# Kernel optimization log

Measured on AMD Instinct MI355X. Metric: run time of the kernel, lower is better.

The kernel has to match this reference:

```python
import jax, jax.numpy as jnp
import numpy as np

N = 50000      # nodes
E = 800000     # edges (before self-loops)
D_IN = 256     # input feature dim
H = 4          # attention heads
C = 32         # per-head channels
HID = H * C    # 128, concat output dim
BN_EPS = 1e-5


def setup_inputs() -> dict:
    key = jax.random.key(0)
    ks = jax.random.split(key, 24)
    inp = {}
    inp["x"] = jax.random.normal(ks[0], (N, D_IN), jnp.float32)
    inp["edge_index"] = jax.random.randint(ks[1], (2, E), 0, N, jnp.int32)
    # layer 1 GATConv params
    inp["W1"] = jax.random.normal(ks[2], (D_IN, HID), jnp.float32) * (2.0 / (D_IN + HID)) ** 0.5
    inp["att_src1"] = jax.random.normal(ks[3], (H, C), jnp.float32) * 0.1
    inp["att_dst1"] = jax.random.normal(ks[4], (H, C), jnp.float32) * 0.1
    inp["bias1"] = jnp.zeros((HID,), jnp.float32)
    # layer 1 BatchNorm (eval mode)
    inp["gamma1"] = 1.0 + 0.1 * jax.random.normal(ks[5], (HID,), jnp.float32)
    inp["beta1"] = 0.1 * jax.random.normal(ks[6], (HID,), jnp.float32)
    inp["mean1"] = 0.1 * jax.random.normal(ks[7], (HID,), jnp.float32)
    inp["var1"] = 0.5 + jax.random.uniform(ks[8], (HID,), jnp.float32)
    # layer 2 GATConv params
    inp["W2"] = jax.random.normal(ks[9], (HID, HID), jnp.float32) * (2.0 / (HID + HID)) ** 0.5
    inp["att_src2"] = jax.random.normal(ks[10], (H, C), jnp.float32) * 0.1
    inp["att_dst2"] = jax.random.normal(ks[11], (H, C), jnp.float32) * 0.1
    inp["bias2"] = jnp.zeros((HID,), jnp.float32)
    # layer 2 BatchNorm (eval mode)
    inp["gamma2"] = 1.0 + 0.1 * jax.random.normal(ks[12], (HID,), jnp.float32)
    inp["beta2"] = 0.1 * jax.random.normal(ks[13], (HID,), jnp.float32)
    inp["mean2"] = 0.1 * jax.random.normal(ks[14], (HID,), jnp.float32)
    inp["var2"] = 0.5 + jax.random.uniform(ks[15], (HID,), jnp.float32)
    return inp


def _gat_layer(x, src, dst, W, att_src, att_dst, bias):
    # x: [N, D]; src/dst: [Etot] with self-loops already appended
    h = (x @ W).reshape(N, H, C)                       # [N, H, C]
    a_s = jnp.einsum("nhc,hc->nh", h, att_src)         # [N, H]
    a_d = jnp.einsum("nhc,hc->nh", h, att_dst)         # [N, H]
    e = jax.nn.leaky_relu(a_s[src] + a_d[dst], 0.2)    # [Etot, H]
    # edge softmax over incoming edges of each destination node
    m = jax.ops.segment_max(e, dst, num_segments=N)    # [N, H]
    ex = jnp.exp(e - m[dst])                           # [Etot, H]
    den = jax.ops.segment_sum(ex, dst, num_segments=N) # [N, H]
    alpha = ex / (den[dst] + 1e-16)                    # [Etot, H]
    out = jax.ops.segment_sum(h[src] * alpha[:, :, None], dst, num_segments=N)
    return out.reshape(N, HID) + bias                  # concat heads + bias


def _bn_eval(x, gamma, beta, mean, var):
    return (x - mean) * (gamma * jax.lax.rsqrt(var + BN_EPS)) + beta


def reference(x, edge_index, W1, att_src1, att_dst1, bias1, gamma1, beta1, mean1, var1,
              W2, att_src2, att_dst2, bias2, gamma2, beta2, mean2, var2):
    loop = jnp.arange(N, dtype=edge_index.dtype)
    src = jnp.concatenate([edge_index[0], loop])  # PyG GATConv adds self-loops
    dst = jnp.concatenate([edge_index[1], loop])
    h = _gat_layer(x, src, dst, W1, att_src1, att_dst1, bias1)
    h = jax.nn.relu(_bn_eval(h, gamma1, beta1, mean1, var1))  # dropout = identity (eval)
    h = _gat_layer(h, src, dst, W2, att_src2, att_dst2, bias2)
    h = jax.nn.relu(_bn_eval(h, gamma2, beta2, mean2, var2))
    return h
```

## Files before the change

kernel.cpp:

```cpp
#include <hip/hip_runtime.h>
#include <math.h>

#define N_NODES 50000
#define EDGES   800000
#define ETOT    (EDGES + N_NODES)
#define HID     128
#define NH      4

typedef __attribute__((ext_vector_type(8))) short short8;
typedef __attribute__((ext_vector_type(4))) float floatx4;

__device__ inline unsigned short f2bf(float f) {
    unsigned int u = __float_as_uint(f);
    u = u + 0x7FFFu + ((u >> 16) & 1u);
    return (unsigned short)(u >> 16);
}

#define NB 391
#define BCAP 2688
#define CHUNK 4096
#define BIN_BLOCKS ((ETOT + CHUNK - 1) / CHUNK)

__global__ __launch_bounds__(256) void init_cursor_kernel(int* __restrict__ cursor) {
    int t = blockIdx.x * 256 + threadIdx.x;
    if (t < NB) cursor[t] = t * BCAP;
}

__global__ __launch_bounds__(256) void bin_scatter_kernel(const int* __restrict__ ei,
                                                          int* __restrict__ cursor,
                                                          int* __restrict__ binned) {
    __shared__ int histL[NB];
    int t = threadIdx.x;
    for (int b = t; b < NB; b += 256) histL[b] = 0;
    __syncthreads();
    int base = blockIdx.x * CHUNK;
    int dreg[16];
#pragma unroll
    for (int j = 0; j < 16; j++) {
        int e = base + j * 256 + t;
        int d = -1;
        if (e < ETOT) d = (e < EDGES) ? ei[EDGES + e] : (e - EDGES);
        dreg[j] = d;
        if (d >= 0) atomicAdd(&histL[d >> 7], 1);
    }
    __syncthreads();
    for (int b = t; b < NB; b += 256) {
        int c = histL[b];
        histL[b] = c ? atomicAdd(&cursor[b], c) : 0;
    }
    __syncthreads();
#pragma unroll
    for (int j = 0; j < 16; j++) {
        int d = dreg[j];
        if (d >= 0) {
            int e = base + j * 256 + t;
            int s = (e < EDGES) ? ei[e] : (e - EDGES);
            int bb = d >> 7;
            int pos = atomicAdd(&histL[bb], 1);
            if (pos < (bb + 1) * BCAP)
                binned[pos] = (s << 7) | (d & 127);
        }
    }
}

__global__ __launch_bounds__(256) void bin_finalize_kernel(const int* __restrict__ binned,
                                                           const int* __restrict__ cursor,
                                                           int* __restrict__ starts,
                                                           int* __restrict__ degs,
                                                           int* __restrict__ csr) {
    __shared__ int histN[128];
    __shared__ int excl[128];
    int b = blockIdx.x, t = threadIdx.x;
    int n0 = b << 7;
    int S = b * BCAP;
    int cnt = cursor[b] - S;
    if (cnt > BCAP) cnt = BCAP;
    if (t < 128) histN[t] = 0;
    __syncthreads();
    for (int j = t; j < cnt; j += 256)
        atomicAdd(&histN[binned[S + j] & 127], 1);
    __syncthreads();
    int v = (t < 128) ? histN[t] : 0;
    if (t < 128) excl[t] = v;
    __syncthreads();
    for (int off = 1; off < 128; off <<= 1) {
        int x = 0, add = 0;
        if (t < 128) { x = excl[t]; if (t >= off) add = excl[t - off]; }
        __syncthreads();
        if (t < 128) excl[t] = x + add;
        __syncthreads();
    }
    if (t < 128) {
        int ex = excl[t] - v;
        int n = n0 + t;
        if (n < N_NODES) { starts[n] = S + ex; degs[n] = v; }
        histN[t] = ex;
    }
    __syncthreads();
    for (int j = t; j < cnt; j += 256) {
        int e = binned[S + j];
        int pos = atomicAdd(&histN[e & 127], 1);
        csr[S + pos] = e >> 7;
    }
}

__global__ void wtrans_coef_kernel(const float* __restrict__ W1, const float* __restrict__ W2,
                                   unsigned short* __restrict__ Wt1, unsigned short* __restrict__ Wt2,
                                   const float* __restrict__ b1, const float* __restrict__ g1,
                                   const float* __restrict__ be1, const float* __restrict__ mn1,
                                   const float* __restrict__ vr1,
                                   const float* __restrict__ b2, const float* __restrict__ g2,
                                   const float* __restrict__ be2, const float* __restrict__ mn2,
                                   const float* __restrict__ vr2, float* __restrict__ coef) {
    int i = blockIdx.x * 256 + threadIdx.x;
    if (i < 256 * 128) { int k = i >> 7, n = i & 127; Wt1[n * 256 + k] = f2bf(W1[i]); }
    if (i < 128 * 128) { int k = i >> 7, n = i & 127; Wt2[n * 128 + k] = f2bf(W2[i]); }
    if (blockIdx.x == 0) {
        int t = threadIdx.x;
        if (t < 128) {
            float sc = g1[t] * rsqrtf(vr1[t] + 1e-5f);
            coef[t]       = sc;
            coef[128 + t] = be1[t] + (b1[t] - mn1[t]) * sc;
        } else {
            int c = t - 128;
            float sc = g2[c] * rsqrtf(vr2[c] + 1e-5f);
            coef[256 + c] = sc;
            coef[384 + c] = be2[c] + (b2[c] - mn2[c]) * sc;
        }
    }
}

#define GR   64
#define KC   64
#define PADK 88
#define PADH 136

union Smem {
    struct { unsigned short Xs[GR][PADK]; unsigned short Ws[HID][PADK]; } s;
    unsigned short Hs[GR][PADH];
};

template<bool XBF16>
__global__ __launch_bounds__(256) void gemm_att_kernel(const void* __restrict__ Xv,
                                                       const unsigned short* __restrict__ Wt,
                                                       const float* __restrict__ att_src,
                                                       const float* __restrict__ att_dst,
                                                       unsigned short* __restrict__ Hout,
                                                       float* __restrict__ aS,
                                                       float* __restrict__ aD, int K) {
    __shared__ Smem sm;
    int t = threadIdx.x, lane = t & 63, w = t >> 6;
    int quad = lane >> 4, nl = lane & 15;
    int rowBase = blockIdx.x * GR;

    floatx4 acc[8];
    floatx4 zero = {0.f, 0.f, 0.f, 0.f};
#pragma unroll
    for (int b = 0; b < 8; b++) acc[b] = zero;

    const float*          Xf = (const float*)Xv;
    const unsigned short* Xb = (const unsigned short*)Xv;

    uint4  xu[2];
    float4 xf[2][2];
    uint4  wu[4];

    auto LOADX = [&](int k0) {
#pragma unroll
        for (int it = 0; it < 2; it++) {
            int s5 = t + it * 256;
            int row = s5 >> 3, kg = s5 & 7;
            int gr = rowBase + row;
            if (XBF16) {
                uint4 v = make_uint4(0, 0, 0, 0);
                if (gr < N_NODES) v = *(const uint4*)&Xb[(unsigned)(gr * K + k0 + kg * 8)];
                xu[it] = v;
            } else {
                float4 v0 = make_float4(0, 0, 0, 0), v1 = v0;
                if (gr < N_NODES) {
                    const float* p = &Xf[(unsigned)(gr * K + k0 + kg * 8)];
                    v0 = *(const float4*)p;
                    v1 = *(const float4*)(p + 4);
                }
                xf[it][0] = v0; xf[it][1] = v1;
            }
        }
    };
    auto LOADW = [&](int k0) {
#pragma unroll
        for (int it = 0; it < 4; it++) {
            int s5 = t + it * 256;
            int nn = s5 >> 3, kg = s5 & 7;
            wu[it] = *(const uint4*)&Wt[(unsigned)(nn * K + k0 + kg * 8)];
        }
    };
    auto STORE = [&]() {
#pragma unroll
        for (int it = 0; it < 2; it++) {
            int s5 = t + it * 256;
            int row = s5 >> 3, kg = s5 & 7;
            if (XBF16) {
                *(uint4*)&sm.s.Xs[row][kg * 8] = xu[it];
            } else {
                unsigned short tmp[8];
                float4 v0 = xf[it][0], v1 = xf[it][1];
                tmp[0] = f2bf(v0.x); tmp[1] = f2bf(v0.y); tmp[2] = f2bf(v0.z); tmp[3] = f2bf(v0.w);
                tmp[4] = f2bf(v1.x); tmp[5] = f2bf(v1.y); tmp[6] = f2bf(v1.z); tmp[7] = f2bf(v1.w);
                *(uint4*)&sm.s.Xs[row][kg * 8] = *(uint4*)tmp;
            }
        }
#pragma unroll
        for (int it = 0; it < 4; it++) {
            int s5 = t + it * 256;
            int nn = s5 >> 3, kg = s5 & 7;
            *(uint4*)&sm.s.Ws[nn][kg * 8] = wu[it];
        }
    };
    auto MFMAC = [&]() {
#pragma unroll
        for (int ks = 0; ks < 2; ks++) {
            int kb = ks * 32 + quad * 8;
            short8 a0 = *(const short8*)&sm.s.Xs[w * 16 + nl][kb];
#pragma unroll
            for (int ct = 0; ct < 8; ct++) {
                short8 b = *(const short8*)&sm.s.Ws[ct * 16 + nl][kb];
                acc[ct] = __builtin_amdgcn_mfma_f32_16x16x32_bf16(a0, b, acc[ct], 0, 0, 0);
            }
        }
    };

    LOADX(0); LOADW(0);
    STORE();
    __syncthreads();
    for (int k0 = KC; k0 < K; k0 += KC) {
        LOADX(k0); LOADW(k0);
        MFMAC();
        __syncthreads();
        STORE();
        __syncthreads();
    }
    MFMAC();
    __syncthreads();

#pragma unroll
    for (int ct = 0; ct < 8; ct++)
#pragma unroll
        for (int r = 0; r < 4; r++)
            sm.Hs[w * 16 + quad * 4 + r][ct * 16 + nl] = f2bf(acc[ct][r]);

    float asv[8], adv[8];
    {
        const float* ap = &att_src[nl * 8];
        const float* dp = &att_dst[nl * 8];
        *(float4*)&asv[0] = *(const float4*)ap;  *(float4*)&asv[4] = *(const float4*)(ap + 4);
        *(float4*)&adv[0] = *(const float4*)dp;  *(float4*)&adv[4] = *(const float4*)(dp + 4);
    }
    int hd = nl >> 2;
#pragma unroll
    for (int it = 0; it < 4; it++) {
        int rl = w * 16 + it * 4 + quad;
        int grow = rowBase + rl;
        uint4 v = *(const uint4*)&sm.Hs[rl][nl * 8];
        float f[8];
        f[0] = __uint_as_float(v.x << 16); f[1] = __uint_as_float(v.x & 0xffff0000u);
        f[2] = __uint_as_float(v.y << 16); f[3] = __uint_as_float(v.y & 0xffff0000u);
        f[4] = __uint_as_float(v.z << 16); f[5] = __uint_as_float(v.z & 0xffff0000u);
        f[6] = __uint_as_float(v.w << 16); f[7] = __uint_as_float(v.w & 0xffff0000u);
        float ds = 0.f, dd = 0.f;
#pragma unroll
        for (int j = 0; j < 8; j++) {
            ds = fmaf(f[j], asv[j], ds);
            dd = fmaf(f[j], adv[j], dd);
        }
        ds += __shfl_xor(ds, 1); ds += __shfl_xor(ds, 2);
        dd += __shfl_xor(dd, 1); dd += __shfl_xor(dd, 2);
        if (grow < N_NODES) {
            *(uint4*)&Hout[(unsigned)(grow * HID + nl * 8)] = v;
            if ((nl & 3) == 0) { aS[grow * 4 + hd] = ds; aD[grow * 4 + hd] = dd; }
        }
    }
}

#define ECAP 64

__device__ __forceinline__ void prefetchR(uint4 (&buf)[4], int sregr, const char* hbase,
                                          int sBase, int l16b) {
#pragma unroll
    for (int u = 0; u < 4; u++) {
        int se = __builtin_amdgcn_ds_bpermute(sBase | (u << 2), sregr);
        buf[u] = *(const uint4*)(hbase + (((long)se) << 8) + l16b);
    }
}

__device__ __forceinline__ void consumeR(const uint4 (&buf)[4], float xrr, int aBase,
                                         float (&acc)[8]) {
#pragma unroll
    for (int u = 0; u < 4; u++) {
        float au = __uint_as_float((unsigned)__builtin_amdgcn_ds_bpermute(
                        aBase | (u << 2), (int)__float_as_uint(xrr)));
        uint4 v = buf[u];
        acc[0] = fmaf(__uint_as_float(v.x << 16),         au, acc[0]);
        acc[1] = fmaf(__uint_as_float(v.x & 0xffff0000u), au, acc[1]);
        acc[2] = fmaf(__uint_as_float(v.y << 16),         au, acc[2]);
        acc[3] = fmaf(__uint_as_float(v.y & 0xffff0000u), au, acc[3]);
        acc[4] = fmaf(__uint_as_float(v.z << 16),         au, acc[4]);
        acc[5] = fmaf(__uint_as_float(v.z & 0xffff0000u), au, acc[5]);
        acc[6] = fmaf(__uint_as_float(v.w << 16),         au, acc[6]);
        acc[7] = fmaf(__uint_as_float(v.w & 0xffff0000u), au, acc[7]);
    }
}

template<bool OUTBF16>
__global__ __launch_bounds__(256) void gather_kernel(const unsigned short* __restrict__ hfeat,
                                                     const float* __restrict__ a_s,
                                                     const float* __restrict__ a_d,
                                                     const int* __restrict__ starts,
                                                     const int* __restrict__ degs,
                                                     const int* __restrict__ csr,
                                                     const float* __restrict__ coefA,
                                                     const float* __restrict__ coefB,
                                                     void* __restrict__ outv) {
    int t = threadIdx.x, lane = t & 63, ws = t >> 6;
    int h = lane >> 4, l16 = lane & 15;
    int n = blockIdx.x * 4 + ws;
    int start = starts[n];
    int deg = degs[n];
    float adh = a_d[(unsigned)(n * 4 + h)];
    const char* hbase = (const char*)hfeat;
    int sBase = lane & 48;
    int aBase = ((lane & 12) << 4) | sBase;
    int l16b = l16 << 4;

    int sreg[4];
#pragma unroll
    for (int it = 0; it < 4; it++) {
        int j = l16 + it * 16;
        sreg[it] = (j < deg) ? csr[start + j] : 0;
    }
    float e[4];
#pragma unroll
    for (int it = 0; it < 4; it++) {
        int j = l16 + it * 16;
        e[it] = -1e30f;
        if (j < deg) {
            float as = a_s[(unsigned)(sreg[it] * 4 + h)];
            float v = as + adh;
            e[it] = v > 0.f ? v : 0.2f * v;
        }
    }

    int cap = deg < ECAP ? deg : ECAP;
    uint4 vA[4], vB[4];
    prefetchR(vA, sreg[0], hbase, sBase, l16b);
    if (cap > 16) prefetchR(vB, sreg[1], hbase, sBase, l16b);

    float m = fmaxf(fmaxf(e[0], e[1]), fmaxf(e[2], e[3]));
    for (int j = ECAP + l16; j < deg; j += 16) {
        int s = csr[start + j];
        float as = a_s[(unsigned)(s * 4 + h)];
        float v = as + adh; v = v > 0.f ? v : 0.2f * v;
        m = fmaxf(m, v);
    }
#pragma unroll
    for (int off = 1; off < 16; off <<= 1) m = fmaxf(m, __shfl_xor(m, off));

    float x[4];
    float d = 0.f;
#pragma unroll
    for (int it = 0; it < 4; it++) { x[it] = __expf(e[it] - m); d += x[it]; }
    for (int j = ECAP + l16; j < deg; j += 16) {
        int s = csr[start + j];
        float as = a_s[(unsigned)(s * 4 + h)];
        float v = as + adh; v = v > 0.f ? v : 0.2f * v;
        d += __expf(v - m);
    }
#pragma unroll
    for (int off = 1; off < 16; off <<= 1) d += __shfl_xor(d, off);
    float rd = 1.0f / (d + 1e-16f);
    float xr[4];
#pragma unroll
    for (int it = 0; it < 4; it++) xr[it] = x[it] * rd;

    float acc[8];
#pragma unroll
    for (int j = 0; j < 8; j++) acc[j] = 0.f;
    consumeR(vA, xr[0], aBase, acc);
    if (cap > 16) {
        if (cap > 32) prefetchR(vA, sreg[2], hbase, sBase, l16b);
        consumeR(vB, xr[1], aBase, acc);
        if (cap > 32) {
            if (cap > 48) prefetchR(vB, sreg[3], hbase, sBase, l16b);
            consumeR(vA, xr[2], aBase, acc);
            if (cap > 48) consumeR(vB, xr[3], aBase, acc);
        }
    }
    if (deg > ECAP) {
        int hh = l16 >> 2;
        int gB = (lane & 12) << 4;
        float mB  = __uint_as_float((unsigned)__builtin_amdgcn_ds_bpermute(gB, (int)__float_as_uint(m)));
        float rdB = __uint_as_float((unsigned)__builtin_amdgcn_ds_bpermute(gB, (int)__float_as_uint(rd)));
        float adhB = a_d[(unsigned)(n * 4 + hh)];
        for (int j = ECAP; j < deg; j++) {
            int s = csr[start + j];
            float asv = a_s[(unsigned)(s * 4 + hh)];
            float v2 = asv + adhB; v2 = v2 > 0.f ? v2 : 0.2f * v2;
            float al = __expf(v2 - mB) * rdB;
            uint4 v = *(const uint4*)(hbase + (((long)s) << 8) + l16b);
            acc[0] = fmaf(__uint_as_float(v.x << 16),         al, acc[0]);
            acc[1] = fmaf(__uint_as_float(v.x & 0xffff0000u), al, acc[1]);
            acc[2] = fmaf(__uint_as_float(v.y << 16),         al, acc[2]);
            acc[3] = fmaf(__uint_as_float(v.y & 0xffff0000u), al, acc[3]);
            acc[4] = fmaf(__uint_as_float(v.z << 16),         al, acc[4]);
            acc[5] = fmaf(__uint_as_float(v.z & 0xffff0000u), al, acc[5]);
            acc[6] = fmaf(__uint_as_float(v.w << 16),         al, acc[6]);
            acc[7] = fmaf(__uint_as_float(v.w & 0xffff0000u), al, acc[7]);
        }
    }

#pragma unroll
    for (int j = 0; j < 8; j++) {
        acc[j] += __shfl_xor(acc[j], 16);
        acc[j] += __shfl_xor(acc[j], 32);
    }

    int g = lane >> 4;
    float o0 = acc[0], o1 = acc[1];
    if (g == 1) { o0 = acc[2]; o1 = acc[3]; }
    if (g == 2) { o0 = acc[4]; o1 = acc[5]; }
    if (g == 3) { o0 = acc[6]; o1 = acc[7]; }
    int c = (l16 << 3) + (g << 1);
    float2 cA = *(const float2*)&coefA[c];
    float2 cB = *(const float2*)&coefB[c];
    float r0 = fmaxf(fmaf(o0, cA.x, cB.x), 0.f);
    float r1 = fmaxf(fmaf(o1, cA.y, cB.y), 0.f);
    unsigned oidx = (unsigned)(n * 64 + (l16 << 2) + g);
    if (OUTBF16) {
        unsigned int pk = (unsigned int)f2bf(r0) | ((unsigned int)f2bf(r1) << 16);
        ((unsigned int*)outv)[oidx] = pk;
    } else {
        ((float2*)outv)[oidx] = make_float2(r0, r1);
    }
}

extern "C" void kernel_launch(void* const* d_in, const int* in_sizes, int n_in,
                              void* d_out, int out_size, void* d_ws, size_t ws_size,
                              hipStream_t stream) {
    const float* x    = (const float*)d_in[0];
    const int*   ei   = (const int*)d_in[1];
    const float* W1   = (const float*)d_in[2];
    const float* as1  = (const float*)d_in[3];
    const float* ad1  = (const float*)d_in[4];
    const float* b1   = (const float*)d_in[5];
    const float* g1   = (const float*)d_in[6];
    const float* be1  = (const float*)d_in[7];
    const float* mn1  = (const float*)d_in[8];
    const float* vr1  = (const float*)d_in[9];
    const float* W2   = (const float*)d_in[10];
    const float* as2  = (const float*)d_in[11];
    const float* ad2  = (const float*)d_in[12];
    const float* b2   = (const float*)d_in[13];
    const float* g2   = (const float*)d_in[14];
    const float* be2  = (const float*)d_in[15];
    const float* mn2  = (const float*)d_in[16];
    const float* vr2  = (const float*)d_in[17];
    float* out = (float*)d_out;

    unsigned short* hb  = (unsigned short*)d_ws;
    unsigned short* x2b = hb + (size_t)N_NODES * HID;
    unsigned short* Wt1 = x2b + (size_t)N_NODES * HID;
    unsigned short* Wt2 = Wt1 + 128 * 256;
    float* aS    = (float*)(Wt2 + 128 * 128);
    float* aD    = aS + N_NODES * NH;
    float* coef  = aD + N_NODES * NH;
    int* cursor  = (int*)(coef + 512);
    int* starts  = cursor + NB;
    int* degs    = starts + N_NODES;
    int* binned  = degs + N_NODES;
    int* csr     = binned + NB * BCAP;

    init_cursor_kernel<<<2, 256, 0, stream>>>(cursor);
    bin_scatter_kernel<<<BIN_BLOCKS, 256, 0, stream>>>(ei, cursor, binned);
    bin_finalize_kernel<<<NB, 256, 0, stream>>>(binned, cursor, starts, degs, csr);
    wtrans_coef_kernel<<<128, 256, 0, stream>>>(W1, W2, Wt1, Wt2,
                                                b1, g1, be1, mn1, vr1,
                                                b2, g2, be2, mn2, vr2, coef);

    int gemmGrid = (N_NODES + GR - 1) / GR;
    int nodeGrid = N_NODES / 4;

    gemm_att_kernel<false><<<gemmGrid, 256, 0, stream>>>(x, Wt1, as1, ad1, hb, aS, aD, 256);
    gather_kernel<true><<<nodeGrid, 256, 0, stream>>>(hb, aS, aD, starts, degs, csr,
                                                      coef, coef + 128, (void*)x2b);
    gemm_att_kernel<true><<<gemmGrid, 256, 0, stream>>>(x2b, Wt2, as2, ad2, hb, aS, aD, 128);
    gather_kernel<false><<<nodeGrid, 256, 0, stream>>>(hb, aS, aD, starts, degs, csr,
                                                       coef + 256, coef + 384, (void*)out);
}
```

Before: 275.5 us.

## Fuse edge binning scatter with layer-1 GEMM into one heterogeneous launch

Merges the edge bin-scatter kernel and the first GEMM+attention kernel into a single launch whose blocks split by index, so the latency-bound atomic scatter can overlap with the compute-bound GEMM. The cursor-init kernel is replaced by a memset, with cursors now relative offsets. The GEMM loses its register prefetch double-buffering and becomes a simple load-sync-compute loop, which shortens register lifetimes but exposes global load latency. Shared memory per block now covers both the GEMM tile and the histogram.

```diff
diff --git a/kernel.cpp b/kernel.cpp
--- a/kernel.cpp
+++ b/kernel.cpp
@@ -21,40 +21,35 @@
 #define CHUNK 4096
 #define BIN_BLOCKS ((ETOT + CHUNK - 1) / CHUNK)
 
-__global__ __launch_bounds__(256) void init_cursor_kernel(int* __restrict__ cursor) {
-    int t = blockIdx.x * 256 + threadIdx.x;
-    if (t < NB) cursor[t] = t * BCAP;
-}
-
-__global__ __launch_bounds__(256) void bin_scatter_kernel(const int* __restrict__ ei,
-                                                          int* __restrict__ cursor,
-                                                          int* __restrict__ binned) {
-    __shared__ int histL[NB];
+__device__ __forceinline__ void bin_scatter_body(int* histL, int bid,
+                                                 const int* __restrict__ ei,
+                                                 int* __restrict__ cursor,
+                                                 int* __restrict__ binned) {
     int t = threadIdx.x;
     for (int b = t; b < NB; b += 256) histL[b] = 0;
     __syncthreads();
-    int base = blockIdx.x * CHUNK;
-    int dreg[16];
+    int base = bid * CHUNK;
 #pragma unroll
     for (int j = 0; j < 16; j++) {
         int e = base + j * 256 + t;
-        int d = -1;
-        if (e < ETOT) d = (e < EDGES) ? ei[EDGES + e] : (e - EDGES);
-        dreg[j] = d;
-        if (d >= 0) atomicAdd(&histL[d >> 7], 1);
+        if (e < ETOT) {
+            int d = (e < EDGES) ? ei[EDGES + e] : (e - EDGES);
+            atomicAdd(&histL[d >> 7], 1);
+        }
     }
     __syncthreads();
     for (int b = t; b < NB; b += 256) {
         int c = histL[b];
-        histL[b] = c ? atomicAdd(&cursor[b], c) : 0;
+        histL[b] = c ? (b * BCAP + atomicAdd(&cursor[b], c)) : 0;
     }
     __syncthreads();
 #pragma unroll
     for (int j = 0; j < 16; j++) {
-        int d = dreg[j];
-        if (d >= 0) {
-            int e = base + j * 256 + t;
-            int s = (e < EDGES) ? ei[e] : (e - EDGES);
+        int e = base + j * 256 + t;
+        if (e < ETOT) {
+            int s, d;
+            if (e < EDGES) { s = ei[e]; d = ei[EDGES + e]; }
+            else           { s = d = e - EDGES; }
             int bb = d >> 7;
             int pos = atomicAdd(&histL[bb], 1);
             if (pos < (bb + 1) * BCAP)
@@ -73,7 +68,7 @@
     int b = blockIdx.x, t = threadIdx.x;
     int n0 = b << 7;
     int S = b * BCAP;
-    int cnt = cursor[b] - S;
+    int cnt = cursor[b];
     if (cnt > BCAP) cnt = BCAP;
     if (t < 128) histN[t] = 0;
     __syncthreads();
@@ -141,17 +136,17 @@
 };
 
 template<bool XBF16>
-__global__ __launch_bounds__(256) void gemm_att_kernel(const void* __restrict__ Xv,
-                                                       const unsigned short* __restrict__ Wt,
-                                                       const float* __restrict__ att_src,
-                                                       const float* __restrict__ att_dst,
-                                                       unsigned short* __restrict__ Hout,
-                                                       float* __restrict__ aS,
-                                                       float* __restrict__ aD, int K) {
-    __shared__ Smem sm;
+__device__ __forceinline__ void gemm_att_body(Smem& sm, int bid,
+                                              const void* __restrict__ Xv,
+                                              const unsigned short* __restrict__ Wt,
+                                              const float* __restrict__ att_src,
+                                              const float* __restrict__ att_dst,
+                                              unsigned short* __restrict__ Hout,
+                                              float* __restrict__ aS,
+                                              float* __restrict__ aD, int K) {
     int t = threadIdx.x, lane = t & 63, w = t >> 6;
     int quad = lane >> 4, nl = lane & 15;
-    int rowBase = blockIdx.x * GR;
+    int rowBase = bid * GR;
 
     floatx4 acc[8];
     floatx4 zero = {0.f, 0.f, 0.f, 0.f};
@@ -161,20 +156,17 @@
     const float*          Xf = (const float*)Xv;
     const unsigned short* Xb = (const unsigned short*)Xv;
 
-    uint4  xu[2];
-    float4 xf[2][2];
-    uint4  wu[4];
-
-    auto LOADX = [&](int k0) {
+    for (int k0 = 0; k0 < K; k0 += KC) {
 #pragma unroll
         for (int it = 0; it < 2; it++) {
             int s5 = t + it * 256;
             int row = s5 >> 3, kg = s5 & 7;
             int gr = rowBase + row;
+            unsigned short tmp[8];
             if (XBF16) {
                 uint4 v = make_uint4(0, 0, 0, 0);
                 if (gr < N_NODES) v = *(const uint4*)&Xb[(unsigned)(gr * K + k0 + kg * 8)];
-                xu[it] = v;
+                *(uint4*)tmp = v;
             } else {
                 float4 v0 = make_float4(0, 0, 0, 0), v1 = v0;
                 if (gr < N_NODES) {
@@ -182,41 +174,18 @@
                     v0 = *(const float4*)p;
                     v1 = *(const float4*)(p + 4);
                 }
-                xf[it][0] = v0; xf[it][1] = v1;
+                tmp[0] = f2bf(v0.x); tmp[1] = f2bf(v0.y); tmp[2] = f2bf(v0.z); tmp[3] = f2bf(v0.w);
+                tmp[4] = f2bf(v1.x); tmp[5] = f2bf(v1.y); tmp[6] = f2bf(v1.z); tmp[7] = f2bf(v1.w);
             }
-        }
-    };
-    auto LOADW = [&](int k0) {
+            *(uint4*)&sm.s.Xs[row][kg * 8] = *(uint4*)tmp;
+        }
 #pragma unroll
         for (int it = 0; it < 4; it++) {
             int s5 = t + it * 256;
-            int nn = s5 >> 3, kg = s5 & 7;
-            wu[it] = *(const uint4*)&Wt[(unsigned)(nn * K + k0 + kg * 8)];
-        }
-    };
-    auto STORE = [&]() {
-#pragma unroll
-        for (int it = 0; it < 2; it++) {
-            int s5 = t + it * 256;
-            int row = s5 >> 3, kg = s5 & 7;
-            if (XBF16) {
-                *(uint4*)&sm.s.Xs[row][kg * 8] = xu[it];
-            } else {
-                unsigned short tmp[8];
-                float4 v0 = xf[it][0], v1 = xf[it][1];
-                tmp[0] = f2bf(v0.x); tmp[1] = f2bf(v0.y); tmp[2] = f2bf(v0.z); tmp[3] = f2bf(v0.w);
-                tmp[4] = f2bf(v1.x); tmp[5] = f2bf(v1.y); tmp[6] = f2bf(v1.z); tmp[7] = f2bf(v1.w);
-                *(uint4*)&sm.s.Xs[row][kg * 8] = *(uint4*)tmp;
-            }
-        }
-#pragma unroll
-        for (int it = 0; it < 4; it++) {
-            int s5 = t + it * 256;
-            int nn = s5 >> 3, kg = s5 & 7;
-            *(uint4*)&sm.s.Ws[nn][kg * 8] = wu[it];
-        }
-    };
-    auto MFMAC = [&]() {
+            int n = s5 >> 3, kg = s5 & 7;
+            *(uint4*)&sm.s.Ws[n][kg * 8] = *(const uint4*)&Wt[(unsigned)(n * K + k0 + kg * 8)];
+        }
+        __syncthreads();
 #pragma unroll
         for (int ks = 0; ks < 2; ks++) {
             int kb = ks * 32 + quad * 8;
@@ -227,20 +196,8 @@
                 acc[ct] = __builtin_amdgcn_mfma_f32_16x16x32_bf16(a0, b, acc[ct], 0, 0, 0);
             }
         }
-    };
-
-    LOADX(0); LOADW(0);
-    STORE();
-    __syncthreads();
-    for (int k0 = KC; k0 < K; k0 += KC) {
-        LOADX(k0); LOADW(k0);
-        MFMAC();
         __syncthreads();
-        STORE();
-        __syncthreads();
-    }
-    MFMAC();
-    __syncthreads();
+    }
 
 #pragma unroll
     for (int ct = 0; ct < 8; ct++)
@@ -279,6 +236,33 @@
             if ((nl & 3) == 0) { aS[grow * 4 + hd] = ds; aD[grow * 4 + hd] = dd; }
         }
     }
+}
+
+__global__ __launch_bounds__(256) void fused_scatter_gemm1(
+        const int* __restrict__ ei, int* __restrict__ cursor, int* __restrict__ binned,
+        const float* __restrict__ x, const unsigned short* __restrict__ Wt1,
+        const float* __restrict__ att_src, const float* __restrict__ att_dst,
+        unsigned short* __restrict__ Hout, float* __restrict__ aS, float* __restrict__ aD) {
+    __shared__ Smem sm;
+    __shared__ int histL[NB];
+    if (blockIdx.x < BIN_BLOCKS) {
+        bin_scatter_body(histL, blockIdx.x, ei, cursor, binned);
+    } else {
+        gemm_att_body<false>(sm, blockIdx.x - BIN_BLOCKS, x, Wt1, att_src, att_dst,
+                             Hout, aS, aD, 256);
+    }
+}
+
+template<bool XBF16>
+__global__ __launch_bounds__(256) void gemm_att_kernel(const void* __restrict__ Xv,
+                                                       const unsigned short* __restrict__ Wt,
+                                                       const float* __restrict__ att_src,
+                                                       const float* __restrict__ att_dst,
+                                                       unsigned short* __restrict__ Hout,
+                                                       float* __restrict__ aS,
+                                                       float* __restrict__ aD, int K) {
+    __shared__ Smem sm;
+    gemm_att_body<XBF16>(sm, blockIdx.x, Xv, Wt, att_src, att_dst, Hout, aS, aD, K);
 }
 
 #define ECAP 64
@@ -478,9 +462,7 @@
     int* binned  = degs + N_NODES;
     int* csr     = binned + NB * BCAP;
 
-    init_cursor_kernel<<<2, 256, 0, stream>>>(cursor);
-    bin_scatter_kernel<<<BIN_BLOCKS, 256, 0, stream>>>(ei, cursor, binned);
-    bin_finalize_kernel<<<NB, 256, 0, stream>>>(binned, cursor, starts, degs, csr);
+    hipMemsetAsync(cursor, 0, NB * sizeof(int), stream);
     wtrans_coef_kernel<<<128, 256, 0, stream>>>(W1, W2, Wt1, Wt2,
                                                 b1, g1, be1, mn1, vr1,
                                                 b2, g2, be2, mn2, vr2, coef);
@@ -488,7 +470,9 @@
     int gemmGrid = (N_NODES + GR - 1) / GR;
     int nodeGrid = N_NODES / 4;
 
-    gemm_att_kernel<false><<<gemmGrid, 256, 0, stream>>>(x, Wt1, as1, ad1, hb, aS, aD, 256);
+    fused_scatter_gemm1<<<BIN_BLOCKS + gemmGrid, 256, 0, stream>>>(
+        ei, cursor, binned, x, Wt1, as1, ad1, hb, aS, aD);
+    bin_finalize_kernel<<<NB, 256, 0, stream>>>(binned, cursor, starts, degs, csr);
     gather_kernel<true><<<nodeGrid, 256, 0, stream>>>(hb, aS, aD, starts, degs, csr,
                                                       coef, coef + 128, (void*)x2b);
     gemm_att_kernel<true><<<gemmGrid, 256, 0, stream>>>(x2b, Wt2, as2, ad2, hb, aS, aD, 128);
```

Result: faster. 248.1 us (-9.9%).
